# Performance work log

Measured on AMD Instinct MI355X. Metric: run time of the kernel, lower is better.

Reference implementation:

```python
import jax, jax.numpy as jnp
import numpy as np

B, N = 2048, 110
H1, F1 = 5, 24   # gat1: 5 heads, 24-dim, concat
H2, F2 = 3, 3    # gat2: 3 heads, 3-dim, average
NEG = -9e15
ALPHA = 0.2  # tf.nn.leaky_relu default alpha


def _glorot(key, shape):
    fan_in, fan_out = shape[-2], shape[-1]
    lim = np.sqrt(6.0 / (fan_in + fan_out))
    return jax.random.uniform(key, shape, jnp.float32, -lim, lim)


def setup_inputs() -> dict:
    key = jax.random.key(0)
    ks = jax.random.split(key, 12)
    X = jax.random.normal(ks[0], (B, N, N), jnp.float32)
    # sparse-ish 0/1 adjacency with self-loops
    A = (jax.random.uniform(ks[1], (B, N, N)) < 0.3).astype(jnp.float32)
    A = jnp.maximum(A, jnp.eye(N, dtype=jnp.float32)[None])
    return {
        "X": X,
        "A": A,
        "M": jax.random.normal(ks[2], (N, N), jnp.float32),  # learnable mask
        "W1": _glorot(ks[3], (H1, N, F1)),
        "as1": _glorot(ks[4], (H1, F1, 1))[..., 0],
        "an1": _glorot(ks[5], (H1, F1, 1))[..., 0],
        "b1": jnp.zeros((F1,), jnp.float32),
        "W2": _glorot(ks[6], (H2, H1 * F1, F2)),
        "as2": _glorot(ks[7], (H2, F2, 1))[..., 0],
        "an2": _glorot(ks[8], (H2, F2, 1))[..., 0],
        "b2": jnp.zeros((F2,), jnp.float32),
        "fc1_w": _glorot(ks[9], (F2, 1)),
        "fc2_w": _glorot(ks[10], (N, N)),
    }


def _gat_layer(X, A, W, a_s, a_n, b, concat):
    # X: [B,N,Din]; W: [H,Din,F]; a_s,a_n: [H,F]; b: [F]
    feats = jnp.einsum('bni,hif->bhnf', X, W)               # per-head projection
    e_s = jnp.einsum('bhnf,hf->bhn', feats, a_s)
    e_n = jnp.einsum('bhnf,hf->bhn', feats, a_n)
    e = jax.nn.leaky_relu(e_s[..., :, None] + e_n[..., None, :], ALPHA)  # [B,H,N,N]
    e = jnp.where(A[:, None] > 0.0, e, NEG)                  # adjacency mask
    attn = jax.nn.softmax(e, axis=-1)
    h = jnp.einsum('bhnm,bhmf->bhnf', attn, feats) + b       # aggregate + bias
    if concat:
        h = jax.nn.leaky_relu(h, ALPHA)
        b_, hh, n_, f_ = h.shape
        return h.transpose(0, 2, 1, 3).reshape(b_, n_, hh * f_)
    # 'average': add heads / H, then activation
    return jax.nn.leaky_relu(h.mean(axis=1), ALPHA)


def reference(X, A, M, W1, as1, an1, b1, W2, as2, an2, b2, fc1_w, fc2_w):
    Xm = X * jax.nn.sigmoid(M)[None]                         # learnable mask gating
    h1 = _gat_layer(Xm, A, W1, as1, an1, b1, concat=True)    # [B,N,H1*F1]
    h2 = _gat_layer(h1, A, W2, as2, an2, b2, concat=False)   # [B,N,F2]
    node_prob = jax.nn.sigmoid(h2 @ fc1_w)                   # [B,N,1]
    t = node_prob.reshape(-1, N)                             # [B,N]
    attn_prob = jax.nn.softmax(t @ fc2_w, axis=-1)           # [B,N]
    return jnp.sum(t * attn_prob, axis=1, keepdims=True)     # [B,1]
```

## Files before the change

### kernel.cpp

```cpp
#include <hip/hip_runtime.h>
#include <math.h>

#define NB 2048
#define NV 110
#define NH1 5
#define NF1 24
#define NH2 3
#define NF2 3
#define C1 (NH1*NF1)
#define LALPHA 0.2f

constexpr int NN = NV*NV;
constexpr int T1 = 1024;
constexpr int KP = 136;
constexpr int W1ROWS = 144;

typedef _Float16 f16;
typedef f16  f16x8 __attribute__((ext_vector_type(8)));
typedef f16  f16x4 __attribute__((ext_vector_type(4)));
typedef __fp16 h16x2 __attribute__((ext_vector_type(2)));
typedef float f32x4 __attribute__((ext_vector_type(4)));

__device__ __forceinline__ f32x4 mfma16(f16x8 a, f16x8 b, f32x4 c) {
  return __builtin_amdgcn_mfma_f32_16x16x32_f16(a, b, c, 0, 0, 0);
}
__device__ __forceinline__ float lrelu(float x){ return x > 0.f ? x : LALPHA*x; }
__device__ __forceinline__ float frcp(float x){ return __builtin_amdgcn_rcpf(x); }
__device__ __forceinline__ float sigm(float x){ return frcp(1.f+__expf(-x)); }
__device__ __forceinline__ float expm4(float v){
  return __builtin_amdgcn_exp2f(fmaf(v, 1.442695041f, -5.770780163f));
}
__device__ __forceinline__ float wmax(float v){
  #pragma unroll
  for (int d=32; d; d>>=1) v = fmaxf(v, __shfl_xor(v,d));
  return v;
}
__device__ __forceinline__ float wsum(float v){
  #pragma unroll
  for (int d=32; d; d>>=1) v += __shfl_xor(v,d);
  return v;
}
__device__ __forceinline__ f32x4 ld4u(const float* p){
  f32x4 v; __builtin_memcpy(&v, p, 16); return v;
}

__global__ void precomp_kernel(const float* __restrict__ M, const float* __restrict__ W1,
                               const float* __restrict__ as1, const float* __restrict__ an1,
                               const float* __restrict__ W2, const float* __restrict__ as2,
                               const float* __restrict__ an2, const float* __restrict__ fc2w,
                               float* __restrict__ Msig, f16* __restrict__ W1tg,
                               f16* __restrict__ W2tg, f16* __restrict__ fc2tg) {
  const int i = blockIdx.x*256 + threadIdx.x;
  if (i < NN) {
    Msig[i] = sigm(M[i]);
  } else if (i < NN + W1ROWS*KP) {
    const int j = i - NN, f = j/KP, k = j%KP;
    float v = 0.f;
    if (k < NV) {
      if (f < C1) {
        v = W1[(f/NF1)*(NV*NF1) + k*NF1 + (f%NF1)];
      } else if (f >= 128 && f < 133) {
        const int h = f - 128;
        for (int ff = 0; ff < NF1; ++ff)
          v += W1[h*(NV*NF1) + k*NF1 + ff] * as1[h*NF1 + ff];
      } else if (f >= 133 && f < 138) {
        const int h = f - 133;
        for (int ff = 0; ff < NF1; ++ff)
          v += W1[h*(NV*NF1) + k*NF1 + ff] * an1[h*NF1 + ff];
      }
    }
    W1tg[f*KP + k] = (f16)v;
  } else if (i < NN + W1ROWS*KP + 16*KP) {
    const int j = i - NN - W1ROWS*KP, r = j/KP, k = j%KP;
    float v = 0.f;
    if (k < C1) {
      if (r < 9) {
        v = W2[(r/NF2)*(C1*NF2) + k*NF2 + (r%NF2)];
      } else if (r < 12) {
        const int g = r - 9;
        for (int f2 = 0; f2 < NF2; ++f2)
          v += W2[g*(C1*NF2) + k*NF2 + f2] * as2[g*NF2 + f2];
      } else if (r < 15) {
        const int g = r - 12;
        for (int f2 = 0; f2 < NF2; ++f2)
          v += W2[g*(C1*NF2) + k*NF2 + f2] * an2[g*NF2 + f2];
      }
    }
    W2tg[r*KP + k] = (f16)v;
  } else if (i < NN + W1ROWS*KP + 16*KP + 112*KP) {
    const int j = i - NN - W1ROWS*KP - 16*KP, col = j/KP, k = j%KP;
    float v = 0.f;
    if (col < NV && k < NV) v = fc2w[k*NV + col];
    fc2tg[col*KP + k] = (f16)v;
  }
}

__global__ __launch_bounds__(T1, 8) void gat_fused(
  const float* __restrict__ X, const float* __restrict__ A,
  const float* __restrict__ Msig, const f16* __restrict__ W1tg,
  const float* __restrict__ b1,  const f16* __restrict__ W2tg,
  const float* __restrict__ b2,  const float* __restrict__ fc1w,
  const f16* __restrict__ fc2tg, float* __restrict__ out)
{
  __shared__ __attribute__((aligned(16))) f16 sXm [112*KP];
  __shared__ __attribute__((aligned(16))) f16 sFt [128*KP];
  __shared__ __attribute__((aligned(16))) f16 sF2t[16*KP];
  __shared__ __attribute__((aligned(16))) float sES [NH1*112];
  __shared__ __attribute__((aligned(16))) float sEN [NH1*128];
  __shared__ __attribute__((aligned(16))) float sES2[NH2*112];
  __shared__ __attribute__((aligned(16))) float sEN2[NH2*128];
  __shared__ unsigned long long sAM[2*112];
  __shared__ __attribute__((aligned(16))) float sHP[112*4];

  const int b = blockIdx.x, tid = threadIdx.x;
  const int wv = tid >> 6, lane = tid & 63;
  const int wq = wv & 7, half = wv >> 3;
  const int lr = lane & 15, lh = lane >> 4;
  const float* __restrict__ Xb = X + (size_t)b*NN;
  const float* __restrict__ Ab = A + (size_t)b*NN;

  float* const sT = sES;
  float* const sS = sES + 128;

  for (int n = tid; n < 110; n += T1) {
    *(unsigned*)&sXm[n*KP + 110] = 0u;
    *(uint4*)&sXm[n*KP + 112] = uint4{0,0,0,0};
    *(uint4*)&sXm[n*KP + 120] = uint4{0,0,0,0};
    *(uint4*)&sXm[n*KP + 128] = uint4{0,0,0,0};
  }
  for (int i = tid; i < 2*KP/8; i += T1)
    ((uint4*)&sXm[110*KP])[i] = uint4{0,0,0,0};
  for (int n = tid; n < 128; n += T1) {
    *(uint4*)&sFt[n*KP + 112] = uint4{0,0,0,0};
    *(uint4*)&sFt[n*KP + 120] = uint4{0,0,0,0};
    *(uint4*)&sFt[n*KP + 128] = uint4{0,0,0,0};
  }
  for (int i = tid; i < (16*KP)/8; i += T1)
    ((uint4*)sF2t)[i] = uint4{0,0,0,0};
  if (tid < 4) sAM[220 + tid] = 0ull;

  for (int t = tid; t < NV*28; t += T1) {
    const int n = t/28, c = t%28, k = 4*c;
    if (c < 27) {
      f32x4 x = ld4u(Xb + n*NV + k);
      f32x4 m = ld4u(Msig + n*NV + k);
      union { f16x4 v4; h16x2 h2[2]; } u;
      u.h2[0] = __builtin_amdgcn_cvt_pkrtz(x[0]*m[0], x[1]*m[1]);
      u.h2[1] = __builtin_amdgcn_cvt_pkrtz(x[2]*m[2], x[3]*m[3]);
      *(f16x4*)&sXm[n*KP + k] = u.v4;
    } else {
      sXm[n*KP + 108] = (f16)(Xb[n*NV+108]*Msig[n*NV+108]);
      sXm[n*KP + 109] = (f16)(Xb[n*NV+109]*Msig[n*NV+109]);
    }
  }
  #pragma unroll
  for (int i = 0; i < 7; ++i) {
    const int n = wv + 16*i;
    if (n < NV) {
      unsigned long long m0 = __ballot(Ab[n*NV + lane] > 0.f);
      const int mm = 64 + lane;
      unsigned long long m1 = __ballot((mm < NV) && (Ab[n*NV + mm] > 0.f));
      if (lane == 0) { sAM[2*n] = m0; sAM[2*n+1] = m1; }
    }
  }
  f16x8 bW[4], bL[4];
  #pragma unroll
  for (int k = 0; k < 4; ++k)
    bW[k] = *(const f16x8*)&W1tg[(wq*16 + lr)*KP + k*32 + lh*8];
  if (half && wq < 7) {
    #pragma unroll
    for (int k = 0; k < 4; ++k)
      bL[k] = *(const f16x8*)&W1tg[(128 + lr)*KP + k*32 + lh*8];
  }
  __syncthreads();

  {
    const int mlo = half ? 4 : 0, mhi = half ? 7 : 4;
    for (int m = mlo; m < mhi; ++m) {
      f32x4 acc = {0.f,0.f,0.f,0.f};
      #pragma unroll
      for (int k = 0; k < 4; ++k) {
        f16x8 af = *(const f16x8*)&sXm[(m*16 + lr)*KP + k*32 + lh*8];
        acc = mfma16(af, bW[k], acc);
      }
      f16x4 v;
      #pragma unroll
      for (int r = 0; r < 4; ++r) v[r] = (f16)acc[r];
      *(f16x4*)&sFt[(wq*16 + lr)*KP + m*16 + lh*4] = v;
    }
    if (half && wq < 7) {
      f32x4 acc = {0.f,0.f,0.f,0.f};
      #pragma unroll
      for (int k = 0; k < 4; ++k) {
        f16x8 af = *(const f16x8*)&sXm[(wq*16 + lr)*KP + k*32 + lh*8];
        acc = mfma16(af, bL[k], acc);
      }
      const int mg0 = wq*16 + lh*4;
      if (lr < 5)       *(f32x4*)&sES[lr*112 + mg0] = acc;
      else if (lr < 10) *(f32x4*)&sEN[(lr-5)*128 + mg0] = acc;
    }
  }
  __syncthreads();

  const int row  = wq*16 + lr;
  const int arow = (row < 112) ? row : 0;
  const unsigned long long am0 = sAM[2*arow], am1 = sAM[2*arow+1];
  const float bvt0 = (lr < NF1) ? b1[lr] : 0.f;
  const float bvt1 = (16 + lr < NF1) ? b1[16 + lr] : 0.f;
  const int np = half ? 2 : 3, pbase = half ? 3 : 0;

  f16 h1r[3][2][4];
  f16x8 pa[4];
  if (wq < 7) {
    #pragma unroll
    for (int pi = 0; pi < 3; ++pi) {
      if (pi < np) {
        const int p = pbase + pi;
        const float es = sES[p*112 + row];
        float psum = 0.f;
        #pragma unroll
        for (int k = 0; k < 4; ++k) {
          const int cb = k*32 + lh*8;
          const f32x4 enA = *(const f32x4*)&sEN[p*128 + cb];
          const f32x4 enB = *(const f32x4*)&sEN[p*128 + cb + 4];
          const unsigned bits = (unsigned)(((cb & 64) ? am1 : am0) >> (cb & 63)) & 0xFFu;
          float e[8];
          #pragma unroll
          for (int j = 0; j < 8; ++j) {
            float v = es + ((j < 4) ? enA[j] : enB[j-4]);
            v = fmaxf(v, LALPHA*v);
            v = (bits & (1u << j)) ? v : -1e30f;
            e[j] = expm4(v);
          }
          psum += ((e[0]+e[1]) + (e[2]+e[3])) + ((e[4]+e[5]) + (e[6]+e[7]));
          union { f16x8 v8; h16x2 h2[4]; } u;
          u.h2[0] = __builtin_amdgcn_cvt_pkrtz(e[0], e[1]);
          u.h2[1] = __builtin_amdgcn_cvt_pkrtz(e[2], e[3]);
          u.h2[2] = __builtin_amdgcn_cvt_pkrtz(e[4], e[5]);
          u.h2[3] = __builtin_amdgcn_cvt_pkrtz(e[6], e[7]);
          pa[k] = u.v8;
        }
        psum += __shfl_xor(psum, 16);
        psum += __shfl_xor(psum, 32);
        f32x4 rs;
        #pragma unroll
        for (int r = 0; r < 4; ++r) rs[r] = __shfl(psum, lh*4 + r);
        #pragma unroll
        for (int nt2 = 0; nt2 < 2; ++nt2) {
          f32x4 acc = {0.f,0.f,0.f,0.f};
          #pragma unroll
          for (int k = 0; k < 4; ++k) {
            f16x8 bf = *(const f16x8*)&sFt[(p*NF1 + nt2*16 + lr)*KP + k*32 + lh*8];
            acc = mfma16(pa[k], bf, acc);
          }
          const float bv = nt2 ? bvt1 : bvt0;
          #pragma unroll
          for (int r = 0; r < 4; ++r)
            h1r[pi][nt2][r] = (f16)lrelu(acc[r]*frcp(rs[r]) + bv);
        }
      }
    }
    #pragma unroll
    for (int pi = 0; pi < 3; ++pi) {
      if (pi < np) {
        const int p = pbase + pi;
        #pragma unroll
        for (int nt2 = 0; nt2 < 2; ++nt2) {
          const int fl = nt2*16 + lr;
          if (fl < NF1) {
            #pragma unroll
            for (int r = 0; r < 4; ++r) {
              const int mg = wq*16 + lh*4 + r;
              if (mg < NV) sXm[mg*KP + p*NF1 + fl] = h1r[pi][nt2][r];
            }
          }
        }
      }
    }
  }
  __syncthreads();

  if (!half && wq < 7) {
    f32x4 acc = {0.f,0.f,0.f,0.f};
    #pragma unroll
    for (int k = 0; k < 4; ++k) {
      f16x8 af = *(const f16x8*)&sXm[(wq*16 + lr)*KP + k*32 + lh*8];
      f16x8 bf = *(const f16x8*)&W2tg[lr*KP + k*32 + lh*8];
      acc = mfma16(af, bf, acc);
    }
    const int mg0 = wq*16 + lh*4;
    if (lr < 9) {
      #pragma unroll
      for (int r = 0; r < 4; ++r) {
        const int mg = mg0 + r;
        if (mg < NV) sF2t[lr*KP + mg] = (f16)acc[r];
      }
    } else if (lr < 12) {
      *(f32x4*)&sES2[(lr-9)*112 + mg0] = acc;
    } else if (lr < 15) {
      *(f32x4*)&sEN2[(lr-12)*128 + mg0] = acc;
    }
  }
  __syncthreads();

  f32x4 a2A = {0.f,0.f,0.f,0.f};
  f32x4 a2B = {0.f,0.f,0.f,0.f};
  float psA = 0.f, psB = 0.f;
  const int ng = half ? 1 : 2, gbase = half ? 2 : 0;
  if (wv == 15 && lane < 18) sT[110 + lane] = 0.f;
  if (wq < 7) {
    #pragma unroll
    for (int gi = 0; gi < 2; ++gi) {
      if (gi < ng) {
        const int g = gbase + gi;
        const float es = sES2[g*112 + row];
        float psum = 0.f;
        #pragma unroll
        for (int k = 0; k < 4; ++k) {
          const int cb = k*32 + lh*8;
          const f32x4 enA = *(const f32x4*)&sEN2[g*128 + cb];
          const f32x4 enB = *(const f32x4*)&sEN2[g*128 + cb + 4];
          const unsigned bits = (unsigned)(((cb & 64) ? am1 : am0) >> (cb & 63)) & 0xFFu;
          float e[8];
          #pragma unroll
          for (int j = 0; j < 8; ++j) {
            float v = es + ((j < 4) ? enA[j] : enB[j-4]);
            v = fmaxf(v, LALPHA*v);
            v = (bits & (1u << j)) ? v : -1e30f;
            e[j] = expm4(v);
          }
          psum += ((e[0]+e[1]) + (e[2]+e[3])) + ((e[4]+e[5]) + (e[6]+e[7]));
          union { f16x8 v8; h16x2 h2[4]; } u;
          u.h2[0] = __builtin_amdgcn_cvt_pkrtz(e[0], e[1]);
          u.h2[1] = __builtin_amdgcn_cvt_pkrtz(e[2], e[3]);
          u.h2[2] = __builtin_amdgcn_cvt_pkrtz(e[4], e[5]);
          u.h2[3] = __builtin_amdgcn_cvt_pkrtz(e[6], e[7]);
          pa[k] = u.v8;
        }
        psum += __shfl_xor(psum, 16);
        psum += __shfl_xor(psum, 32);
        if (gi == 0) psA = psum; else psB = psum;
        const int brow = (lr < NF2) ? (g*NF2 + lr) : 15;
        #pragma unroll
        for (int k = 0; k < 4; ++k) {
          f16x8 bf = *(const f16x8*)&sF2t[brow*KP + k*32 + lh*8];
          if (gi == 0) a2A = mfma16(pa[k], bf, a2A);
          else         a2B = mfma16(pa[k], bf, a2B);
        }
      }
    }
  }
  if (half && wq < 7) {
    #pragma unroll
    for (int r = 0; r < 4; ++r) {
      const int mg = wq*16 + lh*4 + r;
      const float rs2 = __shfl(psA, lh*4 + r);
      if (lr < NF2 && mg < NV) sHP[mg*4 + lr] = a2A[r]*frcp(rs2);
    }
  }
  __syncthreads();

  if (!half && wq < 7) {
    const float fcv = (lr < NF2) ? fc1w[lr] : 0.f;
    const float b2v = (lr < NF2) ? b2[lr]  : 0.f;
    #pragma unroll
    for (int r = 0; r < 4; ++r) {
      const int mg = wq*16 + lh*4 + r;
      const float rs0 = __shfl(psA, lh*4 + r);
      const float rs1 = __shfl(psB, lh*4 + r);
      float hsum = a2A[r]*frcp(rs0) + a2B[r]*frcp(rs1);
      if (lr < NF2 && mg < NV) hsum += sHP[mg*4 + lr];
      float hv = (lr < NF2) ? lrelu(hsum*(1.f/NH2) + b2v)*fcv : 0.f;
      hv += __shfl_xor(hv, 1);
      hv += __shfl_xor(hv, 2);
      hv += __shfl_xor(hv, 4);
      hv += __shfl_xor(hv, 8);
      if (lr == 0 && mg < NV) sT[mg] = sigm(hv);
    }
  }
  __syncthreads();

  if (!half && wq < 7) {
    f32x4 acc = {0.f,0.f,0.f,0.f};
    #pragma unroll
    for (int k = 0; k < 4; ++k) {
      const int cb = k*32 + lh*8;
      const f32x4 tA = *(const f32x4*)&sT[cb];
      const f32x4 tB = *(const f32x4*)&sT[cb + 4];
      union { f16x8 v8; h16x2 h2[4]; } u;
      u.h2[0] = __builtin_amdgcn_cvt_pkrtz(tA[0], tA[1]);
      u.h2[1] = __builtin_amdgcn_cvt_pkrtz(tA[2], tA[3]);
      u.h2[2] = __builtin_amdgcn_cvt_pkrtz(tB[0], tB[1]);
      u.h2[3] = __builtin_amdgcn_cvt_pkrtz(tB[2], tB[3]);
      f16x8 bf = *(const f16x8*)&fc2tg[(wq*16 + lr)*KP + k*32 + lh*8];
      acc = mfma16(u.v8, bf, acc);
    }
    const int col = wq*16 + lr;
    if (lh == 0 && col < NV) sS[col] = acc[0];
  }
  __syncthreads();
  if (wv == 0) {
    const float s0 = sS[lane];
    const float s1 = (64+lane < NV) ? sS[64+lane] : -1e38f;
    const float mx = wmax(fmaxf(s0, s1));
    const float p0 = __expf(s0 - mx);
    const float p1 = (64+lane < NV) ? __expf(s1 - mx) : 0.f;
    const float sum = wsum(p0 + p1);
    float val = sT[lane]*p0 + ((64+lane < NV) ? sT[64+lane]*p1 : 0.f);
    val = wsum(val);
    if (lane == 0) out[b] = val*frcp(sum);
  }
}

extern "C" void kernel_launch(void* const* d_in, const int* in_sizes, int n_in,
                              void* d_out, int out_size, void* d_ws, size_t ws_size,
                              hipStream_t stream) {
  const float* X   = (const float*)d_in[0];
  const float* A   = (const float*)d_in[1];
  const float* M   = (const float*)d_in[2];
  const float* W1  = (const float*)d_in[3];
  const float* as1 = (const float*)d_in[4];
  const float* an1 = (const float*)d_in[5];
  const float* b1  = (const float*)d_in[6];
  const float* W2  = (const float*)d_in[7];
  const float* as2 = (const float*)d_in[8];
  const float* an2 = (const float*)d_in[9];
  const float* b2  = (const float*)d_in[10];
  const float* fc1 = (const float*)d_in[11];
  const float* fc2 = (const float*)d_in[12];
  float* out = (float*)d_out;

  float* Msig = (float*)d_ws;
  f16* W1tg  = (f16*)((char*)d_ws + 48400);
  f16* W2tg  = (f16*)((char*)d_ws + 48400 + W1ROWS*KP*2);
  f16* fc2tg = (f16*)((char*)d_ws + 48400 + W1ROWS*KP*2 + 16*KP*2);

  const int pre_items = NN + W1ROWS*KP + 16*KP + 112*KP;
  precomp_kernel<<<(pre_items + 255)/256, 256, 0, stream>>>(
      M, W1, as1, an1, W2, as2, an2, fc2, Msig, W1tg, W2tg, fc2tg);
  gat_fused<<<NB, T1, 0, stream>>>(X, A, Msig, W1tg, b1, W2tg,
                                   b2, fc1, fc2tg, out);
}
```

Before: 182.5 us.

## Shrink block to 14 waves and remap layer-1 projection onto them

Cuts the block from 16 to 14 waves so no wave sits idle during the attention phases. The lost feature-row tile (rows 112-127) is now produced by an extra MFMA tile on the second-half waves, while the first half produces the attention-logit rows. The per-head h1 results are written straight to shared memory instead of being held in a register array, and the head loops are no longer unrolled, to lower register pressure. The trade-off is less parallelism during the projection phase and more serial work per wave.

```diff
diff --git a/kernel.cpp b/kernel.cpp
--- a/kernel.cpp
+++ b/kernel.cpp
@@ -11,7 +11,7 @@
 #define LALPHA 0.2f
 
 constexpr int NN = NV*NV;
-constexpr int T1 = 1024;
+constexpr int T1 = 896;
 constexpr int KP = 136;
 constexpr int W1ROWS = 144;
 
@@ -95,7 +95,7 @@
   }
 }
 
-__global__ __launch_bounds__(T1, 8) void gat_fused(
+__global__ __launch_bounds__(T1, 7) void gat_fused(
   const float* __restrict__ X, const float* __restrict__ A,
   const float* __restrict__ Msig, const f16* __restrict__ W1tg,
   const float* __restrict__ b1,  const f16* __restrict__ W2tg,
@@ -114,7 +114,8 @@
 
   const int b = blockIdx.x, tid = threadIdx.x;
   const int wv = tid >> 6, lane = tid & 63;
-  const int wq = wv & 7, half = wv >> 3;
+  const int half = (wv >= 7) ? 1 : 0;
+  const int wq = wv - half*7;
   const int lr = lane & 15, lh = lane >> 4;
   const float* __restrict__ Xb = X + (size_t)b*NN;
   const float* __restrict__ Ab = A + (size_t)b*NN;
@@ -154,8 +155,8 @@
     }
   }
   #pragma unroll
-  for (int i = 0; i < 7; ++i) {
-    const int n = wv + 16*i;
+  for (int i = 0; i < 8; ++i) {
+    const int n = wv + 14*i;
     if (n < NV) {
       unsigned long long m0 = __ballot(Ab[n*NV + lane] > 0.f);
       const int mm = 64 + lane;
@@ -163,14 +164,14 @@
       if (lane == 0) { sAM[2*n] = m0; sAM[2*n+1] = m1; }
     }
   }
-  f16x8 bW[4], bL[4];
-  #pragma unroll
-  for (int k = 0; k < 4; ++k)
-    bW[k] = *(const f16x8*)&W1tg[(wq*16 + lr)*KP + k*32 + lh*8];
-  if (half && wq < 7) {
-    #pragma unroll
-    for (int k = 0; k < 4; ++k)
-      bL[k] = *(const f16x8*)&W1tg[(128 + lr)*KP + k*32 + lh*8];
+  f16x8 bW[4], bE[4];
+  {
+    const int browE = half ? (112 + lr) : (128 + lr);
+    #pragma unroll
+    for (int k = 0; k < 4; ++k) {
+      bW[k] = *(const f16x8*)&W1tg[(wq*16 + lr)*KP + k*32 + lh*8];
+      bE[k] = *(const f16x8*)&W1tg[browE*KP + k*32 + lh*8];
+    }
   }
   __syncthreads();
 
@@ -188,13 +189,18 @@
       for (int r = 0; r < 4; ++r) v[r] = (f16)acc[r];
       *(f16x4*)&sFt[(wq*16 + lr)*KP + m*16 + lh*4] = v;
     }
-    if (half && wq < 7) {
-      f32x4 acc = {0.f,0.f,0.f,0.f};
-      #pragma unroll
-      for (int k = 0; k < 4; ++k) {
-        f16x8 af = *(const f16x8*)&sXm[(wq*16 + lr)*KP + k*32 + lh*8];
-        acc = mfma16(af, bL[k], acc);
-      }
+    f32x4 acc = {0.f,0.f,0.f,0.f};
+    #pragma unroll
+    for (int k = 0; k < 4; ++k) {
+      f16x8 af = *(const f16x8*)&sXm[(wq*16 + lr)*KP + k*32 + lh*8];
+      acc = mfma16(af, bE[k], acc);
+    }
+    if (half) {
+      f16x4 v;
+      #pragma unroll
+      for (int r = 0; r < 4; ++r) v[r] = (f16)acc[r];
+      *(f16x4*)&sFt[(112 + lr)*KP + wq*16 + lh*4] = v;
+    } else {
       const int mg0 = wq*16 + lh*4;
       if (lr < 5)       *(f32x4*)&sES[lr*112 + mg0] = acc;
       else if (lr < 10) *(f32x4*)&sEN[(lr-5)*128 + mg0] = acc;
@@ -202,77 +208,62 @@
   }
   __syncthreads();
 
-  const int row  = wq*16 + lr;
-  const int arow = (row < 112) ? row : 0;
-  const unsigned long long am0 = sAM[2*arow], am1 = sAM[2*arow+1];
+  const int row = wq*16 + lr;
+  const unsigned long long am0 = sAM[2*row], am1 = sAM[2*row+1];
   const float bvt0 = (lr < NF1) ? b1[lr] : 0.f;
   const float bvt1 = (16 + lr < NF1) ? b1[16 + lr] : 0.f;
-  const int np = half ? 2 : 3, pbase = half ? 3 : 0;
-
-  f16 h1r[3][2][4];
+
   f16x8 pa[4];
-  if (wq < 7) {
-    #pragma unroll
-    for (int pi = 0; pi < 3; ++pi) {
-      if (pi < np) {
-        const int p = pbase + pi;
-        const float es = sES[p*112 + row];
-        float psum = 0.f;
+  {
+    const int np = half ? 2 : 3, pbase = half ? 3 : 0;
+    #pragma unroll 1
+    for (int pi = 0; pi < np; ++pi) {
+      const int p = pbase + pi;
+      const float es = sES[p*112 + row];
+      float psum = 0.f;
+      #pragma unroll
+      for (int k = 0; k < 4; ++k) {
+        const int cb = k*32 + lh*8;
+        const f32x4 enA = *(const f32x4*)&sEN[p*128 + cb];
+        const f32x4 enB = *(const f32x4*)&sEN[p*128 + cb + 4];
+        const unsigned bits = (unsigned)(((cb & 64) ? am1 : am0) >> (cb & 63)) & 0xFFu;
+        float e[8];
+        #pragma unroll
+        for (int j = 0; j < 8; ++j) {
+          float v = es + ((j < 4) ? enA[j] : enB[j-4]);
+          v = fmaxf(v, LALPHA*v);
+          v = (bits & (1u << j)) ? v : -1e30f;
+          e[j] = expm4(v);
+        }
+        psum += ((e[0]+e[1]) + (e[2]+e[3])) + ((e[4]+e[5]) + (e[6]+e[7]));
+        union { f16x8 v8; h16x2 h2[4]; } u;
+        u.h2[0] = __builtin_amdgcn_cvt_pkrtz(e[0], e[1]);
+        u.h2[1] = __builtin_amdgcn_cvt_pkrtz(e[2], e[3]);
+        u.h2[2] = __builtin_amdgcn_cvt_pkrtz(e[4], e[5]);
+        u.h2[3] = __builtin_amdgcn_cvt_pkrtz(e[6], e[7]);
+        pa[k] = u.v8;
+      }
+      psum += __shfl_xor(psum, 16);
+      psum += __shfl_xor(psum, 32);
+      f32x4 rs;
+      #pragma unroll
+      for (int r = 0; r < 4; ++r) rs[r] = __shfl(psum, lh*4 + r);
+      #pragma unroll
+      for (int nt2 = 0; nt2 < 2; ++nt2) {
+        f32x4 acc = {0.f,0.f,0.f,0.f};
         #pragma unroll
         for (int k = 0; k < 4; ++k) {
-          const int cb = k*32 + lh*8;
-          const f32x4 enA = *(const f32x4*)&sEN[p*128 + cb];
-          const f32x4 enB = *(const f32x4*)&sEN[p*128 + cb + 4];
-          const unsigned bits = (unsigned)(((cb & 64) ? am1 : am0) >> (cb & 63)) & 0xFFu;
-          float e[8];
+          f16x8 bf = *(const f16x8*)&sFt[(p*NF1 + nt2*16 + lr)*KP + k*32 + lh*8];
+          acc = mfma16(pa[k], bf, acc);
+        }
+        const int fl = nt2*16 + lr;
+        const float bv = nt2 ? bvt1 : bvt0;
+        if (fl < NF1) {
           #pragma unroll
-          for (int j = 0; j < 8; ++j) {
-            float v = es + ((j < 4) ? enA[j] : enB[j-4]);
-            v = fmaxf(v, LALPHA*v);
-            v = (bits & (1u << j)) ? v : -1e30f;
-            e[j] = expm4(v);
-          }
-          psum += ((e[0]+e[1]) + (e[2]+e[3])) + ((e[4]+e[5]) + (e[6]+e[7]));
-          union { f16x8 v8; h16x2 h2[4]; } u;
-          u.h2[0] = __builtin_amdgcn_cvt_pkrtz(e[0], e[1]);
-          u.h2[1] = __builtin_amdgcn_cvt_pkrtz(e[2], e[3]);
-          u.h2[2] = __builtin_amdgcn_cvt_pkrtz(e[4], e[5]);
-          u.h2[3] = __builtin_amdgcn_cvt_pkrtz(e[6], e[7]);
-          pa[k] = u.v8;
-        }
-        psum += __shfl_xor(psum, 16);
-        psum += __shfl_xor(psum, 32);
-        f32x4 rs;
-        #pragma unroll
-        for (int r = 0; r < 4; ++r) rs[r] = __shfl(psum, lh*4 + r);
-        #pragma unroll
-        for (int nt2 = 0; nt2 < 2; ++nt2) {
-          f32x4 acc = {0.f,0.f,0.f,0.f};
-          #pragma unroll
-          for (int k = 0; k < 4; ++k) {
-            f16x8 bf = *(const f16x8*)&sFt[(p*NF1 + nt2*16 + lr)*KP + k*32 + lh*8];
-            acc = mfma16(pa[k], bf, acc);
-          }
-          const float bv = nt2 ? bvt1 : bvt0;
-          #pragma unroll
-          for (int r = 0; r < 4; ++r)
-            h1r[pi][nt2][r] = (f16)lrelu(acc[r]*frcp(rs[r]) + bv);
-        }
-      }
-    }
-    #pragma unroll
-    for (int pi = 0; pi < 3; ++pi) {
-      if (pi < np) {
-        const int p = pbase + pi;
-        #pragma unroll
-        for (int nt2 = 0; nt2 < 2; ++nt2) {
-          const int fl = nt2*16 + lr;
-          if (fl < NF1) {
-            #pragma unroll
-            for (int r = 0; r < 4; ++r) {
-              const int mg = wq*16 + lh*4 + r;
-              if (mg < NV) sXm[mg*KP + p*NF1 + fl] = h1r[pi][nt2][r];
-            }
+          for (int r = 0; r < 4; ++r) {
+            const int mg = wq*16 + lh*4 + r;
+            if (mg < NV)
+              sXm[mg*KP + p*NF1 + fl] = (f16)lrelu(acc[r]*frcp(rs[r]) + bv);
           }
         }
       }
@@ -280,7 +271,7 @@
   }
   __syncthreads();
 
-  if (!half && wq < 7) {
+  if (!half) {
     f32x4 acc = {0.f,0.f,0.f,0.f};
     #pragma unroll
     for (int k = 0; k < 4; ++k) {
@@ -306,51 +297,48 @@
   f32x4 a2A = {0.f,0.f,0.f,0.f};
   f32x4 a2B = {0.f,0.f,0.f,0.f};
   float psA = 0.f, psB = 0.f;
-  const int ng = half ? 1 : 2, gbase = half ? 2 : 0;
-  if (wv == 15 && lane < 18) sT[110 + lane] = 0.f;
-  if (wq < 7) {
-    #pragma unroll
-    for (int gi = 0; gi < 2; ++gi) {
-      if (gi < ng) {
-        const int g = gbase + gi;
-        const float es = sES2[g*112 + row];
-        float psum = 0.f;
+  {
+    const int ng = half ? 1 : 2, gbase = half ? 2 : 0;
+    #pragma unroll 1
+    for (int gi = 0; gi < ng; ++gi) {
+      const int g = gbase + gi;
+      const float es = sES2[g*112 + row];
+      float psum = 0.f;
+      #pragma unroll
+      for (int k = 0; k < 4; ++k) {
+        const int cb = k*32 + lh*8;
+        const f32x4 enA = *(const f32x4*)&sEN2[g*128 + cb];
+        const f32x4 enB = *(const f32x4*)&sEN2[g*128 + cb + 4];
+        const unsigned bits = (unsigned)(((cb & 64) ? am1 : am0) >> (cb & 63)) & 0xFFu;
+        float e[8];
         #pragma unroll
-        for (int k = 0; k < 4; ++k) {
-          const int cb = k*32 + lh*8;
-          const f32x4 enA = *(const f32x4*)&sEN2[g*128 + cb];
-          const f32x4 enB = *(const f32x4*)&sEN2[g*128 + cb + 4];
-          const unsigned bits = (unsigned)(((cb & 64) ? am1 : am0) >> (cb & 63)) & 0xFFu;
-          float e[8];
-          #pragma unroll
-          for (int j = 0; j < 8; ++j) {
-            float v = es + ((j < 4) ? enA[j] : enB[j-4]);
-            v = fmaxf(v, LALPHA*v);
-            v = (bits & (1u << j)) ? v : -1e30f;
-            e[j] = expm4(v);
-          }
-          psum += ((e[0]+e[1]) + (e[2]+e[3])) + ((e[4]+e[5]) + (e[6]+e[7]));
-          union { f16x8 v8; h16x2 h2[4]; } u;
-          u.h2[0] = __builtin_amdgcn_cvt_pkrtz(e[0], e[1]);
-          u.h2[1] = __builtin_amdgcn_cvt_pkrtz(e[2], e[3]);
-          u.h2[2] = __builtin_amdgcn_cvt_pkrtz(e[4], e[5]);
-          u.h2[3] = __builtin_amdgcn_cvt_pkrtz(e[6], e[7]);
-          pa[k] = u.v8;
+        for (int j = 0; j < 8; ++j) {
+          float v = es + ((j < 4) ? enA[j] : enB[j-4]);
+          v = fmaxf(v, LALPHA*v);
+          v = (bits & (1u << j)) ? v : -1e30f;
+          e[j] = expm4(v);
         }
-        psum += __shfl_xor(psum, 16);
-        psum += __shfl_xor(psum, 32);
-        if (gi == 0) psA = psum; else psB = psum;
-        const int brow = (lr < NF2) ? (g*NF2 + lr) : 15;
-        #pragma unroll
-        for (int k = 0; k < 4; ++k) {
-          f16x8 bf = *(const f16x8*)&sF2t[brow*KP + k*32 + lh*8];
-          if (gi == 0) a2A = mfma16(pa[k], bf, a2A);
-          else         a2B = mfma16(pa[k], bf, a2B);
-        }
-      }
-    }
-  }
-  if (half && wq < 7) {
+        psum += ((e[0]+e[1]) + (e[2]+e[3])) + ((e[4]+e[5]) + (e[6]+e[7]));
+        union { f16x8 v8; h16x2 h2[4]; } u;
+        u.h2[0] = __builtin_amdgcn_cvt_pkrtz(e[0], e[1]);
+        u.h2[1] = __builtin_amdgcn_cvt_pkrtz(e[2], e[3]);
+        u.h2[2] = __builtin_amdgcn_cvt_pkrtz(e[4], e[5]);
+        u.h2[3] = __builtin_amdgcn_cvt_pkrtz(e[6], e[7]);
+        pa[k] = u.v8;
+      }
+      psum += __shfl_xor(psum, 16);
+      psum += __shfl_xor(psum, 32);
+      if (gi == 0) psA = psum; else psB = psum;
+      const int brow = (lr < NF2) ? (g*NF2 + lr) : 15;
+      #pragma unroll
+      for (int k = 0; k < 4; ++k) {
+        f16x8 bf = *(const f16x8*)&sF2t[brow*KP + k*32 + lh*8];
+        if (gi == 0) a2A = mfma16(pa[k], bf, a2A);
+        else         a2B = mfma16(pa[k], bf, a2B);
+      }
+    }
+  }
+  if (half) {
     #pragma unroll
     for (int r = 0; r < 4; ++r) {
       const int mg = wq*16 + lh*4 + r;
@@ -358,9 +346,10 @@
       if (lr < NF2 && mg < NV) sHP[mg*4 + lr] = a2A[r]*frcp(rs2);
     }
   }
-  __syncthreads();
-
-  if (!half && wq < 7) {
+  if (wv == 13 && lane < 18) sT[110 + lane] = 0.f;
+  __syncthreads();
+
+  if (!half) {
     const float fcv = (lr < NF2) ? fc1w[lr] : 0.f;
     const float b2v = (lr < NF2) ? b2[lr]  : 0.f;
     #pragma unroll
@@ -380,7 +369,7 @@
   }
   __syncthreads();
 
-  if (!half && wq < 7) {
+  if (!half) {
     f32x4 acc = {0.f,0.f,0.f,0.f};
     #pragma unroll
     for (int k = 0; k < 4; ++k) {
```

Result: slower. 225.2 us (+23.4%).
